# Optimization experiments

Measured on AMD Instinct MI355X. Metric: run time of the kernel, lower is better.

## Reference

```python
import jax, jax.numpy as jnp
import numpy as np

B, W, WIN_IN = 8, 2048, 1024
D, NH, DFF, L, KS = 512, 8, 2048, 4, 4
NGENES, G = 20000, 2048


def _ln(x, g, b, eps=1e-5):
    m = jnp.mean(x, -1, keepdims=True)
    v = jnp.var(x, -1, keepdims=True)
    return (x - m) * jax.lax.rsqrt(v + eps) * g + b


def _mha(q_in, kv_in, qkv_w, qkv_b, out_w, out_b, nh):
    d = q_in.shape[-1]
    hd = d // nh
    wq, wk, wv = qkv_w[:d], qkv_w[d:2 * d], qkv_w[2 * d:]
    bq, bk, bv = qkv_b[:d], qkv_b[d:2 * d], qkv_b[2 * d:]
    q = (q_in @ wq.T + bq).reshape(q_in.shape[0], q_in.shape[1], nh, hd)
    k = (kv_in @ wk.T + bk).reshape(kv_in.shape[0], kv_in.shape[1], nh, hd)
    v = (kv_in @ wv.T + bv).reshape(kv_in.shape[0], kv_in.shape[1], nh, hd)
    scores = jnp.einsum('bqhd,bkhd->bhqk', q, k) / jnp.sqrt(jnp.asarray(hd, q.dtype))
    a = jax.nn.softmax(scores, axis=-1)
    o = jnp.einsum('bhqk,bkhd->bqhd', a, v).reshape(q_in.shape[0], q_in.shape[1], d)
    return o @ out_w.T + out_b


def _posenc(S, d, dtype):
    pos = jnp.arange(S, dtype=jnp.float32)[:, None]
    div = jnp.exp(jnp.arange(0, d, 2, dtype=jnp.float32) * (-np.log(10000.0) / d))
    pe = jnp.zeros((S, d), jnp.float32)
    pe = pe.at[:, 0::2].set(jnp.sin(pos * div)).at[:, 1::2].set(jnp.cos(pos * div))
    return pe.astype(dtype)


def setup_inputs():
    key = jax.random.key(0)
    ks_ = jax.random.split(key, 12)

    def n(k, shape, s=0.02):
        return jax.random.normal(k, shape, jnp.float32) * s

    return dict(
        windows=jax.random.normal(ks_[0], (B, W, WIN_IN), jnp.float32),
        gene_ids=jax.random.randint(ks_[1], (G,), 0, NGENES),
        W_window=n(ks_[2], (D, WIN_IN)),
        enc_qkv_w=n(ks_[3], (L, 3 * D, D)),
        enc_qkv_b=jnp.zeros((L, 3 * D), jnp.float32),
        enc_out_w=n(ks_[4], (L, D, D)),
        enc_out_b=jnp.zeros((L, D), jnp.float32),
        enc_ln1_g=jnp.ones((L, D), jnp.float32),
        enc_ln1_b=jnp.zeros((L, D), jnp.float32),
        enc_ln2_g=jnp.ones((L, D), jnp.float32),
        enc_ln2_b=jnp.zeros((L, D), jnp.float32),
        enc_ff1_w=n(ks_[5], (L, DFF, D)),
        enc_ff1_b=jnp.zeros((L, DFF), jnp.float32),
        enc_ff2_w=n(ks_[6], (L, D, DFF)),
        enc_ff2_b=jnp.zeros((L, D), jnp.float32),
        gene_embed=n(ks_[7], (NGENES, D), 1.0),
        ca_qkv_w=n(ks_[8], (3 * D, D)),
        ca_qkv_b=jnp.zeros((3 * D,), jnp.float32),
        ca_out_w=n(ks_[9], (D, D)),
        ca_out_b=jnp.zeros((D,), jnp.float32),
        ro_ln_g=jnp.ones((D,), jnp.float32),
        ro_ln_b=jnp.zeros((D,), jnp.float32),
        ro_w=n(ks_[10], (1, D)),
        ro_b=jnp.zeros((1,), jnp.float32),
    )


def reference(windows, gene_ids, W_window, enc_qkv_w, enc_qkv_b, enc_out_w,
              enc_out_b, enc_ln1_g, enc_ln1_b, enc_ln2_g, enc_ln2_b,
              enc_ff1_w, enc_ff1_b, enc_ff2_w, enc_ff2_b, gene_embed,
              ca_qkv_w, ca_qkv_b, ca_out_w, ca_out_b, ro_ln_g, ro_ln_b,
              ro_w, ro_b):
    # proj_window (Linear, no bias; dropout inactive in eval)
    x = windows @ W_window.T                          # [B, W, D]
    Bn, Wn, _ = x.shape
    # AvgPool1d(kernel=stride=KS) along the window axis
    x = x.reshape(Bn, Wn // KS, KS, D).mean(axis=2)   # [B, S, D]
    S = x.shape[1]
    x = x + _posenc(S, D, x.dtype)[None]
    # pre-LN TransformerEncoder, relu FFN, no final norm
    for i in range(L):
        h = _ln(x, enc_ln1_g[i], enc_ln1_b[i])
        x = x + _mha(h, h, enc_qkv_w[i], enc_qkv_b[i], enc_out_w[i], enc_out_b[i], NH)
        h = _ln(x, enc_ln2_g[i], enc_ln2_b[i])
        x = x + (jax.nn.relu(h @ enc_ff1_w[i].T + enc_ff1_b[i]) @ enc_ff2_w[i].T + enc_ff2_b[i])
    # gene queries -> cross attention over encoded windows
    q = jnp.broadcast_to(gene_embed[gene_ids][None], (Bn, gene_ids.shape[0], D))
    z = _mha(q, x, ca_qkv_w, ca_qkv_b, ca_out_w, ca_out_b, NH)   # [B, G, D]
    pred = (_ln(z, ro_ln_g, ro_ln_b) @ ro_w.T + ro_b)[..., 0]    # [B, G]
    return pred, z
```

## Files before the change

### kernel.cpp

```cpp
#include <hip/hip_runtime.h>
#include <math.h>


typedef __attribute__((ext_vector_type(8))) short short8v;
typedef __attribute__((ext_vector_type(4))) float float4v;
typedef const __attribute__((address_space(1))) void* gas_t;
typedef __attribute__((address_space(3))) void* las_t;

__device__ inline unsigned short f2bf(float f) {
    unsigned int u = __builtin_bit_cast(unsigned int, f);
    return (unsigned short)((u + 0x7fffu + ((u >> 16) & 1u)) >> 16);
}

__device__ inline unsigned cvt_pk_bf16(float lo, float hi) {
    unsigned r;
    asm("v_cvt_pk_bf16_f32 %0, %1, %2" : "=v"(r) : "v"(lo), "v"(hi));
    return r;
}

__global__ __launch_bounds__(256) void cvt_k(const float* __restrict__ src,
                                             unsigned short* __restrict__ dst, int n4)
{
    int i = blockIdx.x * 256 + threadIdx.x;
    if (i >= n4) return;
    float4 v = ((const float4*)src)[i];
    ushort4 o;
    o.x = f2bf(v.x); o.y = f2bf(v.y); o.z = f2bf(v.z); o.w = f2bf(v.w);
    ((ushort4*)dst)[i] = o;
}

__global__ __launch_bounds__(256) void pool_windows_k(const float* __restrict__ win,
                                                      unsigned short* __restrict__ pw)
{
    int idx = blockIdx.x * 256 + threadIdx.x;
    int n = idx >> 8, c4 = (idx & 255) << 2;
    const float* base = win + (size_t)n * 4096 + c4;
    float4 a = *(const float4*)(base);
    float4 b2 = *(const float4*)(base + 1024);
    float4 c = *(const float4*)(base + 2048);
    float4 d = *(const float4*)(base + 3072);
    ushort4 r;
    r.x = f2bf((a.x + b2.x + c.x + d.x) * 0.25f);
    r.y = f2bf((a.y + b2.y + c.y + d.y) * 0.25f);
    r.z = f2bf((a.z + b2.z + c.z + d.z) * 0.25f);
    r.w = f2bf((a.w + b2.w + c.w + d.w) * 0.25f);
    ((ushort4*)pw)[idx] = r;
}

template<int BM, bool BIAS, bool BROW, bool RES, bool RELU, bool POSENC, bool O32, bool O16>
__global__ __launch_bounds__(256) void gemm_bf16_k(
    const unsigned short* __restrict__ A, const unsigned short* __restrict__ Bw,
    const float* __restrict__ bias, const float* __restrict__ Res,
    float* __restrict__ C32, unsigned short* __restrict__ C16,
    int M, int N, int K)
{
    constexpr int WC   = (BM == 128) ? 2 : 4;
    constexpr int NSTEP = 128 / WC;
    constexpr int MFR  = 4;
    constexpr int NFR  = NSTEP / 16;
    __shared__ __align__(16) unsigned short As[BM * 32];
    __shared__ __align__(16) unsigned short Bs[128 * 32];
    const int tid = threadIdx.x;
    const int lane = tid & 63;
    const int n0 = blockIdx.x * 128, m0 = blockIdx.y * BM;
    const int wr = (BM == 128) ? (tid >> 7) : 0;
    const int wc = (tid >> 6) & (WC - 1);
    const unsigned short* gA0 = A + (size_t)(m0 + (tid >> 2)) * K + (tid & 3) * 8;
    const unsigned short* gA1 = A + (size_t)(m0 + (tid >> 2) + 64) * K + (tid & 3) * 8;
    const unsigned short* gB0 = Bw + (size_t)(n0 + (tid >> 2)) * K + (tid & 3) * 8;
    const unsigned short* gB1 = Bw + (size_t)(n0 + (tid >> 2) + 64) * K + (tid & 3) * 8;
    const int r = lane & 15, g = lane >> 4;
    const int aoff = (64 * wr + r) * 32 + g * 8;
    const int boff = (NSTEP * wc + r) * 32 + g * 8;

    float4v acc[MFR][NFR];
    float4v z4 = {0.f, 0.f, 0.f, 0.f};
    #pragma unroll
    for (int i = 0; i < MFR; ++i)
        #pragma unroll
        for (int j = 0; j < NFR; ++j) acc[i][j] = z4;

    for (int k0 = 0; k0 < K; k0 += 32) {
        __builtin_amdgcn_global_load_lds((gas_t)(gA0 + k0), (las_t)(&As[tid * 8]), 16, 0, 0);
        if constexpr (BM == 128)
            __builtin_amdgcn_global_load_lds((gas_t)(gA1 + k0), (las_t)(&As[(tid + 256) * 8]), 16, 0, 0);
        __builtin_amdgcn_global_load_lds((gas_t)(gB0 + k0), (las_t)(&Bs[tid * 8]), 16, 0, 0);
        __builtin_amdgcn_global_load_lds((gas_t)(gB1 + k0), (las_t)(&Bs[(tid + 256) * 8]), 16, 0, 0);
        __syncthreads();
        short8v a[MFR], b[NFR];
        #pragma unroll
        for (int mi = 0; mi < MFR; ++mi) a[mi] = *(const short8v*)&As[aoff + mi * (16 * 32)];
        #pragma unroll
        for (int ni = 0; ni < NFR; ++ni) b[ni] = *(const short8v*)&Bs[boff + ni * (16 * 32)];
        #pragma unroll
        for (int mi = 0; mi < MFR; ++mi)
            #pragma unroll
            for (int ni = 0; ni < NFR; ++ni)
                acc[mi][ni] = __builtin_amdgcn_mfma_f32_16x16x32_bf16(a[mi], b[ni], acc[mi][ni], 0, 0, 0);
        __syncthreads();
    }

    #pragma unroll
    for (int mi = 0; mi < MFR; ++mi) {
        #pragma unroll
        for (int ni = 0; ni < NFR; ++ni) {
            const int row0 = m0 + 64 * wr + 16 * mi + g * 4;
            const int col  = n0 + NSTEP * wc + 16 * ni + r;
            float bv = (BIAS && !BROW) ? bias[col] : 0.f;
            float fr = 0.f;
            if (POSENC) fr = __expf((float)(col & ~1) * -0.01798894600f);
            #pragma unroll
            for (int q = 0; q < 4; ++q) {
                const int row = row0 + q;
                float v = acc[mi][ni][q] + bv;
                if (BIAS && BROW) v += bias[row];
                if (POSENC) {
                    float ang = (float)(row & 511) * fr;
                    v += (col & 1) ? __cosf(ang) : __sinf(ang);
                }
                if (RES) v += Res[(size_t)row * N + col];
                if (RELU) v = fmaxf(v, 0.f);
                if (O32) C32[(size_t)row * N + col] = v;
                if (O16) C16[(size_t)row * N + col] = f2bf(v);
            }
        }
    }
}

__global__ __launch_bounds__(256) void flashb_k(
    const unsigned short* __restrict__ Qp, long long q_bs, int q_rs,
    const unsigned short* __restrict__ Kp, long long k_bs, int k_rs,
    const unsigned short* __restrict__ Vtp, long long v_hs, long long v_bs, int v_rs,
    unsigned short* __restrict__ Op, long long o_bs, int o_rs, int skv)
{
    constexpr float C1 = 0.18033688011112042f;
    __shared__ __align__(16) unsigned short Ks[64 * 72];
    __shared__ __align__(16) unsigned short Vs[64 * 72];
    __shared__ __align__(16) unsigned short Ps[64 * 72];
    const int qt = blockIdx.x, h = blockIdx.y, b = blockIdx.z;
    const unsigned short* Q  = Qp  + (size_t)b * q_bs + (size_t)h * 64;
    const unsigned short* K  = Kp  + (size_t)b * k_bs + (size_t)h * 64;
    const unsigned short* Vt = Vtp + (size_t)h * v_hs + (size_t)b * v_bs;
    unsigned short* O = Op + (size_t)b * o_bs + (size_t)h * 64;
    const int q0 = qt * 64;
    const int tid = threadIdx.x, lane = tid & 63, w = tid >> 6;
    const int r = lane & 15, g = lane >> 4;

    const unsigned short* qrow = Q + (size_t)(q0 + 16 * w + r) * q_rs + g * 8;
    short8v qf0 = *(const short8v*)(qrow);
    short8v qf1 = *(const short8v*)(qrow + 32);

    const int sr0 = tid >> 3, sr1 = sr0 + 32, sc0 = (tid & 7) * 8;
    const unsigned short* Krow0 = K + (size_t)sr0 * k_rs + sc0;
    const unsigned short* Krow1 = K + (size_t)sr1 * k_rs + sc0;
    const unsigned short* Vrow0 = Vt + (size_t)sr0 * v_rs + sc0;
    const unsigned short* Vrow1 = Vt + (size_t)sr1 * v_rs + sc0;

    uint4 pk0 = *(const uint4*)(Krow0);
    uint4 pk1 = *(const uint4*)(Krow1);
    uint4 pv0 = *(const uint4*)(Vrow0);
    uint4 pv1 = *(const uint4*)(Vrow1);

    float4v acc_o[4];
    float4v z4 = {0.f, 0.f, 0.f, 0.f};
    #pragma unroll
    for (int dt = 0; dt < 4; ++dt) acc_o[dt] = z4;
    float m_own = -INFINITY, l_own = 0.f;

    for (int kv0 = 0; kv0 < skv; kv0 += 64) {
        __syncthreads();
        *(uint4*)&Ks[sr0 * 72 + sc0] = pk0;
        *(uint4*)&Ks[sr1 * 72 + sc0] = pk1;
        *(uint4*)&Vs[sr0 * 72 + sc0] = pv0;
        *(uint4*)&Vs[sr1 * 72 + sc0] = pv1;
        __syncthreads();
        const int kvn = kv0 + 64;
        if (kvn < skv) {
            pk0 = *(const uint4*)(Krow0 + (size_t)kvn * k_rs);
            pk1 = *(const uint4*)(Krow1 + (size_t)kvn * k_rs);
            pv0 = *(const uint4*)(Vrow0 + kvn);
            pv1 = *(const uint4*)(Vrow1 + kvn);
        }

        float4v accs[4];
        #pragma unroll
        for (int t = 0; t < 4; ++t) {
            accs[t] = z4;
            short8v kf0 = *(const short8v*)&Ks[(16 * t + r) * 72 + g * 8];
            short8v kf1 = *(const short8v*)&Ks[(16 * t + r) * 72 + 32 + g * 8];
            accs[t] = __builtin_amdgcn_mfma_f32_16x16x32_bf16(kf0, qf0, accs[t], 0, 0, 0);
            accs[t] = __builtin_amdgcn_mfma_f32_16x16x32_bf16(kf1, qf1, accs[t], 0, 0, 0);
        }

        float sm = accs[0][0];
        #pragma unroll
        for (int t = 0; t < 4; ++t)
            #pragma unroll
            for (int j = 0; j < 4; ++j) sm = fmaxf(sm, accs[t][j]);
        sm = fmaxf(sm, __shfl_xor(sm, 16));
        sm = fmaxf(sm, __shfl_xor(sm, 32));

        if (__any(sm > m_own + 64.f)) {
            float mn = fmaxf(m_own, sm);
            float alpha = __builtin_amdgcn_exp2f((m_own - mn) * C1);
            m_own = mn;
            float a0_ = __shfl(alpha, g * 4 + 0);
            float a1_ = __shfl(alpha, g * 4 + 1);
            float a2_ = __shfl(alpha, g * 4 + 2);
            float a3_ = __shfl(alpha, g * 4 + 3);
            #pragma unroll
            for (int dt = 0; dt < 4; ++dt) {
                acc_o[dt][0] *= a0_; acc_o[dt][1] *= a1_;
                acc_o[dt][2] *= a2_; acc_o[dt][3] *= a3_;
            }
            l_own *= alpha;
        }

        const float m2 = m_own * C1;
        float p[4][4];
        float rsum = 0.f;
        #pragma unroll
        for (int t = 0; t < 4; ++t)
            #pragma unroll
            for (int j = 0; j < 4; ++j) {
                float pv = __builtin_amdgcn_exp2f(__builtin_fmaf(accs[t][j], C1, -m2));
                p[t][j] = pv; rsum += pv;
            }
        rsum += __shfl_xor(rsum, 16);
        rsum += __shfl_xor(rsum, 32);
        l_own += rsum;

        #pragma unroll
        for (int t = 0; t < 4; ++t) {
            uint2 uu;
            uu.x = cvt_pk_bf16(p[t][0], p[t][1]);
            uu.y = cvt_pk_bf16(p[t][2], p[t][3]);
            *(uint2*)&Ps[(16 * w + r) * 72 + 16 * t + g * 4] = uu;
        }

        short8v pf0 = *(const short8v*)&Ps[(16 * w + r) * 72 + g * 8];
        short8v pf1 = *(const short8v*)&Ps[(16 * w + r) * 72 + 32 + g * 8];
        #pragma unroll
        for (int dt = 0; dt < 4; ++dt) {
            short8v vf0 = *(const short8v*)&Vs[(16 * dt + r) * 72 + g * 8];
            short8v vf1 = *(const short8v*)&Vs[(16 * dt + r) * 72 + 32 + g * 8];
            acc_o[dt] = __builtin_amdgcn_mfma_f32_16x16x32_bf16(pf0, vf0, acc_o[dt], 0, 0, 0);
            acc_o[dt] = __builtin_amdgcn_mfma_f32_16x16x32_bf16(pf1, vf1, acc_o[dt], 0, 0, 0);
        }
    }

    float il0 = 1.f / __shfl(l_own, g * 4 + 0);
    float il1 = 1.f / __shfl(l_own, g * 4 + 1);
    float il2 = 1.f / __shfl(l_own, g * 4 + 2);
    float il3 = 1.f / __shfl(l_own, g * 4 + 3);
    #pragma unroll
    for (int dt = 0; dt < 4; ++dt) {
        O[(size_t)(q0 + 16 * w + g * 4 + 0) * o_rs + 16 * dt + r] = f2bf(acc_o[dt][0] * il0);
        O[(size_t)(q0 + 16 * w + g * 4 + 1) * o_rs + 16 * dt + r] = f2bf(acc_o[dt][1] * il1);
        O[(size_t)(q0 + 16 * w + g * 4 + 2) * o_rs + 16 * dt + r] = f2bf(acc_o[dt][2] * il2);
        O[(size_t)(q0 + 16 * w + g * 4 + 3) * o_rs + 16 * dt + r] = f2bf(acc_o[dt][3] * il3);
    }
}

__global__ __launch_bounds__(64) void ln_k(const float* __restrict__ X, unsigned short* __restrict__ Y,
                                           const float* __restrict__ g, const float* __restrict__ bt)
{
    int row = blockIdx.x, lane = threadIdx.x;
    const float* x = X + (size_t)row * 512;
    int c0 = lane * 4, c1 = 256 + lane * 4;
    float4 a0 = *(const float4*)&x[c0];
    float4 a1 = *(const float4*)&x[c1];
    float s  = a0.x + a0.y + a0.z + a0.w + a1.x + a1.y + a1.z + a1.w;
    float ss = a0.x * a0.x + a0.y * a0.y + a0.z * a0.z + a0.w * a0.w
             + a1.x * a1.x + a1.y * a1.y + a1.z * a1.z + a1.w * a1.w;
    #pragma unroll
    for (int off = 1; off < 64; off <<= 1) { s += __shfl_xor(s, off); ss += __shfl_xor(ss, off); }
    float mean = s * (1.f / 512.f);
    float var  = ss * (1.f / 512.f) - mean * mean;
    float rs = rsqrtf(var + 1e-5f);
    float4 g0 = *(const float4*)&g[c0], g1 = *(const float4*)&g[c1];
    float4 b0 = *(const float4*)&bt[c0], b1 = *(const float4*)&bt[c1];
    unsigned short* y = Y + (size_t)row * 512;
    ushort4 o0, o1;
    o0.x = f2bf((a0.x - mean) * rs * g0.x + b0.x);  o0.y = f2bf((a0.y - mean) * rs * g0.y + b0.y);
    o0.z = f2bf((a0.z - mean) * rs * g0.z + b0.z);  o0.w = f2bf((a0.w - mean) * rs * g0.w + b0.w);
    o1.x = f2bf((a1.x - mean) * rs * g1.x + b1.x);  o1.y = f2bf((a1.y - mean) * rs * g1.y + b1.y);
    o1.z = f2bf((a1.z - mean) * rs * g1.z + b1.z);  o1.w = f2bf((a1.w - mean) * rs * g1.w + b1.w);
    *(ushort4*)&y[c0] = o0;
    *(ushort4*)&y[c1] = o1;
}

__global__ __launch_bounds__(128) void gather_k(const float* __restrict__ ge, const int* __restrict__ ids,
                                                unsigned short* __restrict__ out)
{
    int gi = blockIdx.x, t = threadIdx.x;
    int id = ids[gi];
    float4 v = *(const float4*)&ge[(size_t)id * 512 + t * 4];
    ushort4 o;
    o.x = f2bf(v.x); o.y = f2bf(v.y); o.z = f2bf(v.z); o.w = f2bf(v.w);
    *(ushort4*)&out[(size_t)gi * 512 + t * 4] = o;
}

__global__ __launch_bounds__(64) void readout_k(const float* __restrict__ Z,
                                                const float* __restrict__ g, const float* __restrict__ bt,
                                                const float* __restrict__ rw, const float* __restrict__ rb,
                                                float* __restrict__ pred)
{
    int row = blockIdx.x, lane = threadIdx.x;
    const float* zr = Z + (size_t)row * 512;
    int c0 = lane * 4, c1 = 256 + lane * 4;
    float4 a0 = *(const float4*)&zr[c0];
    float4 a1 = *(const float4*)&zr[c1];
    float s  = a0.x + a0.y + a0.z + a0.w + a1.x + a1.y + a1.z + a1.w;
    float ss = a0.x * a0.x + a0.y * a0.y + a0.z * a0.z + a0.w * a0.w
             + a1.x * a1.x + a1.y * a1.y + a1.z * a1.z + a1.w * a1.w;
    #pragma unroll
    for (int off = 1; off < 64; off <<= 1) { s += __shfl_xor(s, off); ss += __shfl_xor(ss, off); }
    float mean = s * (1.f / 512.f);
    float var  = ss * (1.f / 512.f) - mean * mean;
    float rs = rsqrtf(var + 1e-5f);
    float4 g0 = *(const float4*)&g[c0], g1 = *(const float4*)&g[c1];
    float4 b0 = *(const float4*)&bt[c0], b1 = *(const float4*)&bt[c1];
    float4 w0 = *(const float4*)&rw[c0], w1 = *(const float4*)&rw[c1];
    float acc = 0.f;
    acc += ((a0.x - mean) * rs * g0.x + b0.x) * w0.x;
    acc += ((a0.y - mean) * rs * g0.y + b0.y) * w0.y;
    acc += ((a0.z - mean) * rs * g0.z + b0.z) * w0.z;
    acc += ((a0.w - mean) * rs * g0.w + b0.w) * w0.w;
    acc += ((a1.x - mean) * rs * g1.x + b1.x) * w1.x;
    acc += ((a1.y - mean) * rs * g1.y + b1.y) * w1.y;
    acc += ((a1.z - mean) * rs * g1.z + b1.z) * w1.z;
    acc += ((a1.w - mean) * rs * g1.w + b1.w) * w1.w;
    #pragma unroll
    for (int off = 1; off < 64; off <<= 1) acc += __shfl_xor(acc, off);
    if (lane == 0) pred[row] = acc + rb[0];
}

extern "C" void kernel_launch(void* const* d_in, const int* in_sizes, int n_in,
                              void* d_out, int out_size, void* d_ws, size_t ws_size,
                              hipStream_t stream)
{
    (void)in_sizes; (void)n_in; (void)out_size; (void)ws_size;
    const float* windows    = (const float*)d_in[0];
    const int*   gene_ids   = (const int*)  d_in[1];
    const float* W_window   = (const float*)d_in[2];
    const float* enc_qkv_w  = (const float*)d_in[3];
    const float* enc_qkv_b  = (const float*)d_in[4];
    const float* enc_out_w  = (const float*)d_in[5];
    const float* enc_out_b  = (const float*)d_in[6];
    const float* enc_ln1_g  = (const float*)d_in[7];
    const float* enc_ln1_b  = (const float*)d_in[8];
    const float* enc_ln2_g  = (const float*)d_in[9];
    const float* enc_ln2_b  = (const float*)d_in[10];
    const float* enc_ff1_w  = (const float*)d_in[11];
    const float* enc_ff1_b  = (const float*)d_in[12];
    const float* enc_ff2_w  = (const float*)d_in[13];
    const float* enc_ff2_b  = (const float*)d_in[14];
    const float* gene_embed = (const float*)d_in[15];
    const float* ca_qkv_w   = (const float*)d_in[16];
    const float* ca_qkv_b   = (const float*)d_in[17];
    const float* ca_out_w   = (const float*)d_in[18];
    const float* ca_out_b   = (const float*)d_in[19];
    const float* ro_ln_g    = (const float*)d_in[20];
    const float* ro_ln_b    = (const float*)d_in[21];
    const float* ro_w       = (const float*)d_in[22];
    const float* ro_b       = (const float*)d_in[23];

    float* pred = (float*)d_out;
    float* z    = pred + (size_t)8 * 2048;

    char* wp = (char*)d_ws;
    float* x = (float*)wp;                       wp += (size_t)4096 * 512 * 4;
    unsigned short* x16   = (unsigned short*)wp; wp += (size_t)4096 * 512 * 2;
    unsigned short* h16   = (unsigned short*)wp; wp += (size_t)4096 * 512 * 2;
    unsigned short* qkv16 = (unsigned short*)wp; wp += (size_t)4096 * 1536 * 2;
    unsigned short* ao16  = (unsigned short*)wp; wp += (size_t)4096 * 512 * 2;
    unsigned short* big16 = (unsigned short*)wp; wp += (size_t)16384 * 512 * 2;
    unsigned short* vt16  = (unsigned short*)wp; wp += (size_t)512 * 4096 * 2;
    unsigned short* wW16     = (unsigned short*)wp; wp += (size_t)512 * 1024 * 2;
    unsigned short* wqkv16   = (unsigned short*)wp; wp += (size_t)4 * 1536 * 512 * 2;
    unsigned short* wout16   = (unsigned short*)wp; wp += (size_t)4 * 512 * 512 * 2;
    unsigned short* wff116   = (unsigned short*)wp; wp += (size_t)4 * 2048 * 512 * 2;
    unsigned short* wff216   = (unsigned short*)wp; wp += (size_t)4 * 512 * 2048 * 2;
    unsigned short* wcaqkv16 = (unsigned short*)wp; wp += (size_t)1536 * 512 * 2;
    unsigned short* wcaout16 = (unsigned short*)wp; wp += (size_t)512 * 512 * 2;
    unsigned short* pw16  = big16;
    unsigned short* ff116 = big16;
    unsigned short* oc16  = big16;
    unsigned short* ge16  = qkv16;
    unsigned short* qg16  = qkv16 + (size_t)2048 * 512;
    unsigned short* kc16  = qkv16 + (size_t)2 * 2048 * 512;

    auto cvt = [&](const float* s, unsigned short* d, int n) {
        cvt_k<<<(n / 4 + 255) / 256, 256, 0, stream>>>(s, d, n / 4);
    };
    cvt(W_window,  wW16,     512 * 1024);
    cvt(enc_qkv_w, wqkv16,   4 * 1536 * 512);
    cvt(enc_out_w, wout16,   4 * 512 * 512);
    cvt(enc_ff1_w, wff116,   4 * 2048 * 512);
    cvt(enc_ff2_w, wff216,   4 * 512 * 2048);
    cvt(ca_qkv_w,  wcaqkv16, 1536 * 512);
    cvt(ca_out_w,  wcaout16, 512 * 512);

    pool_windows_k<<<4096, 256, 0, stream>>>(windows, pw16);
    gemm_bf16_k<64, false, false, false, false, true, true, false><<<dim3(4, 64), 256, 0, stream>>>(
        pw16, wW16, nullptr, nullptr, x, nullptr, 4096, 512, 1024);

    for (int l = 0; l < 4; ++l) {
        const unsigned short* wl = wqkv16 + (size_t)l * 1536 * 512;
        ln_k<<<4096, 64, 0, stream>>>(x, h16, enc_ln1_g + l * 512, enc_ln1_b + l * 512);
        gemm_bf16_k<128, true, false, false, false, false, false, true><<<dim3(8, 32), 256, 0, stream>>>(
            h16, wl, enc_qkv_b + l * 1536, nullptr, nullptr, qkv16, 4096, 1024, 512);
        gemm_bf16_k<64, true, true, false, false, false, false, true><<<dim3(32, 8), 256, 0, stream>>>(
            wl + (size_t)1024 * 512, h16, enc_qkv_b + l * 1536 + 1024, nullptr,
            nullptr, vt16, 512, 4096, 512);
        flashb_k<<<dim3(8, 8, 8), 256, 0, stream>>>(
            qkv16, (long long)512 * 1024, 1024,
            qkv16 + 512, (long long)512 * 1024, 1024,
            vt16, (long long)64 * 4096, 512LL, 4096,
            ao16, (long long)512 * 512, 512, 512);
        gemm_bf16_k<64, true, false, true, false, false, true, false><<<dim3(4, 64), 256, 0, stream>>>(
            ao16, wout16 + (size_t)l * 512 * 512, enc_out_b + l * 512, x, x, nullptr, 4096, 512, 512);
        ln_k<<<4096, 64, 0, stream>>>(x, h16, enc_ln2_g + l * 512, enc_ln2_b + l * 512);
        gemm_bf16_k<128, true, false, false, true, false, false, true><<<dim3(16, 32), 256, 0, stream>>>(
            h16, wff116 + (size_t)l * 2048 * 512, enc_ff1_b + l * 2048, nullptr,
            nullptr, ff116, 4096, 2048, 512);
        if (l == 3)
            gemm_bf16_k<64, true, false, true, false, false, true, true><<<dim3(4, 64), 256, 0, stream>>>(
                ff116, wff216 + (size_t)l * 512 * 2048, enc_ff2_b + l * 512, x, x, x16, 4096, 512, 2048);
        else
            gemm_bf16_k<64, true, false, true, false, false, true, false><<<dim3(4, 64), 256, 0, stream>>>(
                ff116, wff216 + (size_t)l * 512 * 2048, enc_ff2_b + l * 512, x, x, nullptr, 4096, 512, 2048);
    }

    gather_k<<<2048, 128, 0, stream>>>(gene_embed, gene_ids, ge16);
    gemm_bf16_k<64, true, false, false, false, false, false, true><<<dim3(4, 32), 256, 0, stream>>>(
        ge16, wcaqkv16, ca_qkv_b, nullptr, nullptr, qg16, 2048, 512, 512);
    gemm_bf16_k<64, true, false, false, false, false, false, true><<<dim3(4, 64), 256, 0, stream>>>(
        x16, wcaqkv16 + (size_t)512 * 512, ca_qkv_b + 512, nullptr, nullptr, kc16, 4096, 512, 512);
    gemm_bf16_k<64, true, true, false, false, false, false, true><<<dim3(32, 8), 256, 0, stream>>>(
        wcaqkv16 + (size_t)1024 * 512, x16, ca_qkv_b + 1024, nullptr, nullptr, vt16, 512, 4096, 512);
    flashb_k<<<dim3(32, 8, 8), 256, 0, stream>>>(
        qg16, 0LL, 512,
        kc16, (long long)512 * 512, 512,
        vt16, (long long)64 * 4096, 512LL, 4096,
        oc16, (long long)2048 * 512, 512, 512);
    gemm_bf16_k<128, true, false, false, false, false, true, false><<<dim3(4, 128), 256, 0, stream>>>(
        oc16, wcaout16, ca_out_b, nullptr, z, nullptr, 16384, 512, 512);

    readout_k<<<16384, 64, 0, stream>>>(z, ro_ln_g, ro_ln_b, ro_w, ro_b, pred);
}
```

Baseline: 616.5 us.

## Split encoder attention over KV halves with combine, double-buffer LDS via direct loads

Replaces the flash attention kernel with a templated version that stages K/V tiles into double-buffered, XOR-swizzled LDS using direct global-to-LDS loads, and raises wave priority around the MFMA sections. For the encoder self-attention, the KV range is split in two across extra blocks to double the grid. A new combine kernel merges the partial outputs using the saved per-row max and sum. This aims to improve occupancy and latency hiding, at the cost of an extra kernel launch and an extra pass over the partial outputs in memory.

```diff
diff --git a/kernel.cpp b/kernel.cpp
--- a/kernel.cpp
+++ b/kernel.cpp
@@ -119,7 +119,7 @@
                     v += (col & 1) ? __cosf(ang) : __sinf(ang);
                 }
                 if (RES) v += Res[(size_t)row * N + col];
-                if (RELU) v = fmaxf(v, 0.f);
+                if (RELU) v = fmaxf(v, 0.0f);
                 if (O32) C32[(size_t)row * N + col] = v;
                 if (O16) C16[(size_t)row * N + col] = f2bf(v);
             }
@@ -127,39 +127,49 @@
     }
 }
 
-__global__ __launch_bounds__(256) void flashb_k(
+template<bool SPLIT>
+__global__ __launch_bounds__(256) void flashc_k(
     const unsigned short* __restrict__ Qp, long long q_bs, int q_rs,
     const unsigned short* __restrict__ Kp, long long k_bs, int k_rs,
     const unsigned short* __restrict__ Vtp, long long v_hs, long long v_bs, int v_rs,
-    unsigned short* __restrict__ Op, long long o_bs, int o_rs, int skv)
+    unsigned short* __restrict__ Op, long long o_bs, int o_rs,
+    unsigned short* __restrict__ opart, float2* __restrict__ Ml,
+    int nsplit, int nc)
 {
     constexpr float C1 = 0.18033688011112042f;
-    __shared__ __align__(16) unsigned short Ks[64 * 72];
-    __shared__ __align__(16) unsigned short Vs[64 * 72];
-    __shared__ __align__(16) unsigned short Ps[64 * 72];
-    const int qt = blockIdx.x, h = blockIdx.y, b = blockIdx.z;
+    __shared__ __align__(16) unsigned short Kb[2][64 * 64];
+    __shared__ __align__(16) unsigned short Vb[2][64 * 64];
+    __shared__ __align__(16) unsigned short Ps[64 * 64];
+    const int qt = blockIdx.x, h = blockIdx.y, z = blockIdx.z;
+    const int b = z / nsplit, s = z - b * nsplit;
     const unsigned short* Q  = Qp  + (size_t)b * q_bs + (size_t)h * 64;
-    const unsigned short* K  = Kp  + (size_t)b * k_bs + (size_t)h * 64;
-    const unsigned short* Vt = Vtp + (size_t)h * v_hs + (size_t)b * v_bs;
-    unsigned short* O = Op + (size_t)b * o_bs + (size_t)h * 64;
+    const unsigned short* Kg = Kp  + (size_t)b * k_bs + (size_t)h * 64 + (size_t)(s * nc * 64) * k_rs;
+    const unsigned short* Vg = Vtp + (size_t)h * v_hs + (size_t)b * v_bs + (size_t)(s * nc) * 64;
     const int q0 = qt * 64;
     const int tid = threadIdx.x, lane = tid & 63, w = tid >> 6;
     const int r = lane & 15, g = lane >> 4;
+    const int sw8 = (r & 7) * 8;
+    const int cA = (g * 8) ^ sw8;
+    const int cB = ((g + 4) * 8) ^ sw8;
 
     const unsigned short* qrow = Q + (size_t)(q0 + 16 * w + r) * q_rs + g * 8;
     short8v qf0 = *(const short8v*)(qrow);
     short8v qf1 = *(const short8v*)(qrow + 32);
 
-    const int sr0 = tid >> 3, sr1 = sr0 + 32, sc0 = (tid & 7) * 8;
-    const unsigned short* Krow0 = K + (size_t)sr0 * k_rs + sc0;
-    const unsigned short* Krow1 = K + (size_t)sr1 * k_rs + sc0;
-    const unsigned short* Vrow0 = Vt + (size_t)sr0 * v_rs + sc0;
-    const unsigned short* Vrow1 = Vt + (size_t)sr1 * v_rs + sc0;
-
-    uint4 pk0 = *(const uint4*)(Krow0);
-    uint4 pk1 = *(const uint4*)(Krow1);
-    uint4 pv0 = *(const uint4*)(Vrow0);
-    uint4 pv1 = *(const uint4*)(Vrow1);
+    const int r0 = tid >> 3, cc = tid & 7;
+    const int srcc = (cc ^ (r0 & 7)) * 8;
+    auto stage = [&](int bi, int c) {
+        const unsigned short* kc_ = Kg + (size_t)c * 64 * k_rs;
+        const unsigned short* vc_ = Vg + (size_t)c * 64;
+        __builtin_amdgcn_global_load_lds((gas_t)(kc_ + (size_t)r0 * k_rs + srcc),
+                                         (las_t)(&Kb[bi][tid * 8]), 16, 0, 0);
+        __builtin_amdgcn_global_load_lds((gas_t)(kc_ + (size_t)(r0 + 32) * k_rs + srcc),
+                                         (las_t)(&Kb[bi][(tid + 256) * 8]), 16, 0, 0);
+        __builtin_amdgcn_global_load_lds((gas_t)(vc_ + (size_t)r0 * v_rs + srcc),
+                                         (las_t)(&Vb[bi][tid * 8]), 16, 0, 0);
+        __builtin_amdgcn_global_load_lds((gas_t)(vc_ + (size_t)(r0 + 32) * v_rs + srcc),
+                                         (las_t)(&Vb[bi][(tid + 256) * 8]), 16, 0, 0);
+    };
 
     float4v acc_o[4];
     float4v z4 = {0.f, 0.f, 0.f, 0.f};
@@ -167,36 +177,33 @@
     for (int dt = 0; dt < 4; ++dt) acc_o[dt] = z4;
     float m_own = -INFINITY, l_own = 0.f;
 
-    for (int kv0 = 0; kv0 < skv; kv0 += 64) {
-        __syncthreads();
-        *(uint4*)&Ks[sr0 * 72 + sc0] = pk0;
-        *(uint4*)&Ks[sr1 * 72 + sc0] = pk1;
-        *(uint4*)&Vs[sr0 * 72 + sc0] = pv0;
-        *(uint4*)&Vs[sr1 * 72 + sc0] = pv1;
-        __syncthreads();
-        const int kvn = kv0 + 64;
-        if (kvn < skv) {
-            pk0 = *(const uint4*)(Krow0 + (size_t)kvn * k_rs);
-            pk1 = *(const uint4*)(Krow1 + (size_t)kvn * k_rs);
-            pv0 = *(const uint4*)(Vrow0 + kvn);
-            pv1 = *(const uint4*)(Vrow1 + kvn);
-        }
-
+    stage(0, 0);
+    __syncthreads();
+    int buf = 0;
+
+    for (int c = 0; c < nc; ++c) {
+        if (c + 1 < nc) stage(buf ^ 1, c + 1);
+        const unsigned short* KL = Kb[buf];
+        const unsigned short* VL = Vb[buf];
+
+        __builtin_amdgcn_s_setprio(1);
         float4v accs[4];
         #pragma unroll
         for (int t = 0; t < 4; ++t) {
             accs[t] = z4;
-            short8v kf0 = *(const short8v*)&Ks[(16 * t + r) * 72 + g * 8];
-            short8v kf1 = *(const short8v*)&Ks[(16 * t + r) * 72 + 32 + g * 8];
+            const unsigned short* krow = KL + (16 * t + r) * 64;
+            short8v kf0 = *(const short8v*)(krow + cA);
+            short8v kf1 = *(const short8v*)(krow + cB);
             accs[t] = __builtin_amdgcn_mfma_f32_16x16x32_bf16(kf0, qf0, accs[t], 0, 0, 0);
             accs[t] = __builtin_amdgcn_mfma_f32_16x16x32_bf16(kf1, qf1, accs[t], 0, 0, 0);
         }
-
-        float sm = accs[0][0];
-        #pragma unroll
-        for (int t = 0; t < 4; ++t)
-            #pragma unroll
-            for (int j = 0; j < 4; ++j) sm = fmaxf(sm, accs[t][j]);
+        __builtin_amdgcn_s_setprio(0);
+
+        float m0_ = fmaxf(fmaxf(accs[0][0], accs[0][1]), fmaxf(accs[0][2], accs[0][3]));
+        float m1_ = fmaxf(fmaxf(accs[1][0], accs[1][1]), fmaxf(accs[1][2], accs[1][3]));
+        float m2_ = fmaxf(fmaxf(accs[2][0], accs[2][1]), fmaxf(accs[2][2], accs[2][3]));
+        float m3_ = fmaxf(fmaxf(accs[3][0], accs[3][1]), fmaxf(accs[3][2], accs[3][3]));
+        float sm = fmaxf(fmaxf(m0_, m1_), fmaxf(m2_, m3_));
         sm = fmaxf(sm, __shfl_xor(sm, 16));
         sm = fmaxf(sm, __shfl_xor(sm, 32));
 
@@ -216,50 +223,99 @@
             l_own *= alpha;
         }
 
-        const float m2 = m_own * C1;
+        const float m2c = m_own * C1;
         float p[4][4];
         float rsum = 0.f;
         #pragma unroll
         for (int t = 0; t < 4; ++t)
             #pragma unroll
             for (int j = 0; j < 4; ++j) {
-                float pv = __builtin_amdgcn_exp2f(__builtin_fmaf(accs[t][j], C1, -m2));
+                float pv = __builtin_amdgcn_exp2f(__builtin_fmaf(accs[t][j], C1, -m2c));
                 p[t][j] = pv; rsum += pv;
             }
         rsum += __shfl_xor(rsum, 16);
         rsum += __shfl_xor(rsum, 32);
         l_own += rsum;
 
+        const int prow = (16 * w + r) * 64;
         #pragma unroll
         for (int t = 0; t < 4; ++t) {
             uint2 uu;
             uu.x = cvt_pk_bf16(p[t][0], p[t][1]);
             uu.y = cvt_pk_bf16(p[t][2], p[t][3]);
-            *(uint2*)&Ps[(16 * w + r) * 72 + 16 * t + g * 4] = uu;
-        }
-
-        short8v pf0 = *(const short8v*)&Ps[(16 * w + r) * 72 + g * 8];
-        short8v pf1 = *(const short8v*)&Ps[(16 * w + r) * 72 + 32 + g * 8];
+            int pc = (((2 * t + (g >> 1)) * 8) ^ sw8) + (g & 1) * 4;
+            *(uint2*)&Ps[prow + pc] = uu;
+        }
+
+        __builtin_amdgcn_s_setprio(1);
+        short8v pf0 = *(const short8v*)&Ps[prow + cA];
+        short8v pf1 = *(const short8v*)&Ps[prow + cB];
         #pragma unroll
         for (int dt = 0; dt < 4; ++dt) {
-            short8v vf0 = *(const short8v*)&Vs[(16 * dt + r) * 72 + g * 8];
-            short8v vf1 = *(const short8v*)&Vs[(16 * dt + r) * 72 + 32 + g * 8];
+            const unsigned short* vrow = VL + (16 * dt + r) * 64;
+            short8v vf0 = *(const short8v*)(vrow + cA);
+            short8v vf1 = *(const short8v*)(vrow + cB);
             acc_o[dt] = __builtin_amdgcn_mfma_f32_16x16x32_bf16(pf0, vf0, acc_o[dt], 0, 0, 0);
             acc_o[dt] = __builtin_amdgcn_mfma_f32_16x16x32_bf16(pf1, vf1, acc_o[dt], 0, 0, 0);
         }
+        __builtin_amdgcn_s_setprio(0);
+
+        __syncthreads();
+        buf ^= 1;
     }
 
     float il0 = 1.f / __shfl(l_own, g * 4 + 0);
     float il1 = 1.f / __shfl(l_own, g * 4 + 1);
     float il2 = 1.f / __shfl(l_own, g * 4 + 2);
     float il3 = 1.f / __shfl(l_own, g * 4 + 3);
-    #pragma unroll
-    for (int dt = 0; dt < 4; ++dt) {
-        O[(size_t)(q0 + 16 * w + g * 4 + 0) * o_rs + 16 * dt + r] = f2bf(acc_o[dt][0] * il0);
-        O[(size_t)(q0 + 16 * w + g * 4 + 1) * o_rs + 16 * dt + r] = f2bf(acc_o[dt][1] * il1);
-        O[(size_t)(q0 + 16 * w + g * 4 + 2) * o_rs + 16 * dt + r] = f2bf(acc_o[dt][2] * il2);
-        O[(size_t)(q0 + 16 * w + g * 4 + 3) * o_rs + 16 * dt + r] = f2bf(acc_o[dt][3] * il3);
+    if (SPLIT) {
+        unsigned short* Ob = opart + ((size_t)(s * 4096 + b * 512)) * 512 + h * 64;
+        #pragma unroll
+        for (int dt = 0; dt < 4; ++dt) {
+            Ob[(size_t)(q0 + 16 * w + g * 4 + 0) * 512 + 16 * dt + r] = f2bf(acc_o[dt][0] * il0);
+            Ob[(size_t)(q0 + 16 * w + g * 4 + 1) * 512 + 16 * dt + r] = f2bf(acc_o[dt][1] * il1);
+            Ob[(size_t)(q0 + 16 * w + g * 4 + 2) * 512 + 16 * dt + r] = f2bf(acc_o[dt][2] * il2);
+            Ob[(size_t)(q0 + 16 * w + g * 4 + 3) * 512 + 16 * dt + r] = f2bf(acc_o[dt][3] * il3);
+        }
+        if (g == 0)
+            Ml[((size_t)(s * 8 + b) * 8 + h) * 512 + q0 + 16 * w + r] = make_float2(m_own, l_own);
+    } else {
+        unsigned short* O = Op + (size_t)b * o_bs + (size_t)h * 64;
+        #pragma unroll
+        for (int dt = 0; dt < 4; ++dt) {
+            O[(size_t)(q0 + 16 * w + g * 4 + 0) * o_rs + 16 * dt + r] = f2bf(acc_o[dt][0] * il0);
+            O[(size_t)(q0 + 16 * w + g * 4 + 1) * o_rs + 16 * dt + r] = f2bf(acc_o[dt][1] * il1);
+            O[(size_t)(q0 + 16 * w + g * 4 + 2) * o_rs + 16 * dt + r] = f2bf(acc_o[dt][2] * il2);
+            O[(size_t)(q0 + 16 * w + g * 4 + 3) * o_rs + 16 * dt + r] = f2bf(acc_o[dt][3] * il3);
+        }
     }
+}
+
+__global__ __launch_bounds__(256) void combine_k(const unsigned short* __restrict__ opart,
+                                                 const float2* __restrict__ Ml,
+                                                 unsigned short* __restrict__ Oo)
+{
+    constexpr float C1 = 0.18033688011112042f;
+    const int row = blockIdx.x;
+    const int b = row >> 9, srow = row & 511;
+    const int tid = threadIdx.x;
+    const int h = tid >> 5, t = tid & 31;
+    float2 ml0 = Ml[((size_t)(0 * 8 + b) * 8 + h) * 512 + srow];
+    float2 ml1 = Ml[((size_t)(1 * 8 + b) * 8 + h) * 512 + srow];
+    float m  = fmaxf(ml0.x, ml1.x);
+    float e0 = __builtin_amdgcn_exp2f((ml0.x - m) * C1) * ml0.y;
+    float e1 = __builtin_amdgcn_exp2f((ml1.x - m) * C1) * ml1.y;
+    float inv = 1.f / (e0 + e1);
+    float w0 = e0 * inv, w1 = e1 * inv;
+    const int col = h * 64 + t * 2;
+    unsigned u0 = *(const unsigned*)&opart[((size_t)0 * 4096 + row) * 512 + col];
+    unsigned u1 = *(const unsigned*)&opart[((size_t)1 * 4096 + row) * 512 + col];
+    float a0 = __builtin_bit_cast(float, (u0 & 0xffffu) << 16);
+    float a1 = __builtin_bit_cast(float, (u0 >> 16) << 16);
+    float c0 = __builtin_bit_cast(float, (u1 & 0xffffu) << 16);
+    float c1 = __builtin_bit_cast(float, (u1 >> 16) << 16);
+    unsigned out = cvt_pk_bf16(w0 * a0 + w1 * c0, w0 * a1 + w1 * c1);
+    *(unsigned*)&Oo[(size_t)row * 512 + col] = out;
 }
 
 __global__ __launch_bounds__(64) void ln_k(const float* __restrict__ X, unsigned short* __restrict__ Y,
@@ -384,9 +440,11 @@
     unsigned short* wff216   = (unsigned short*)wp; wp += (size_t)4 * 512 * 2048 * 2;
     unsigned short* wcaqkv16 = (unsigned short*)wp; wp += (size_t)1536 * 512 * 2;
     unsigned short* wcaout16 = (unsigned short*)wp; wp += (size_t)512 * 512 * 2;
-    unsigned short* pw16  = big16;
-    unsigned short* ff116 = big16;
-    unsigned short* oc16  = big16;
+    unsigned short* pw16   = big16;
+    unsigned short* ff116  = big16;
+    unsigned short* oc16   = big16;
+    unsigned short* opart16 = big16;
+    float2* mlbuf = (float2*)(big16 + (size_t)2 * 4096 * 512);
     unsigned short* ge16  = qkv16;
     unsigned short* qg16  = qkv16 + (size_t)2048 * 512;
     unsigned short* kc16  = qkv16 + (size_t)2 * 2048 * 512;
@@ -414,11 +472,13 @@
         gemm_bf16_k<64, true, true, false, false, false, false, true><<<dim3(32, 8), 256, 0, stream>>>(
             wl + (size_t)1024 * 512, h16, enc_qkv_b + l * 1536 + 1024, nullptr,
             nullptr, vt16, 512, 4096, 512);
-        flashb_k<<<dim3(8, 8, 8), 256, 0, stream>>>(
+        flashc_k<true><<<dim3(8, 8, 16), 256, 0, stream>>>(
             qkv16, (long long)512 * 1024, 1024,
             qkv16 + 512, (long long)512 * 1024, 1024,
             vt16, (long long)64 * 4096, 512LL, 4096,
-            ao16, (long long)512 * 512, 512, 512);
+            nullptr, 0LL, 0,
+            opart16, mlbuf, 2, 4);
+        combine_k<<<4096, 256, 0, stream>>>(opart16, mlbuf, ao16);
         gemm_bf16_k<64, true, false, true, false, false, true, false><<<dim3(4, 64), 256, 0, stream>>>(
             ao16, wout16 + (size_t)l * 512 * 512, enc_out_b + l * 512, x, x, nullptr, 4096, 512, 512);
         ln_k<<<4096, 64, 0, stream>>>(x, h16, enc_ln2_g + l * 512, enc_ln2_b + l * 512);
@@ -440,11 +500,12 @@
         x16, wcaqkv16 + (size_t)512 * 512, ca_qkv_b + 512, nullptr, nullptr, kc16, 4096, 512, 512);
     gemm_bf16_k<64, true, true, false, false, false, false, true><<<dim3(32, 8), 256, 0, stream>>>(
         wcaqkv16 + (size_t)1024 * 512, x16, ca_qkv_b + 1024, nullptr, nullptr, vt16, 512, 4096, 512);
-    flashb_k<<<dim3(32, 8, 8), 256, 0, stream>>>(
+    flashc_k<false><<<dim3(32, 8, 8), 256, 0, stream>>>(
         qg16, 0LL, 512,
         kc16, (long long)512 * 512, 512,
         vt16, (long long)64 * 4096, 512LL, 4096,
-        oc16, (long long)2048 * 512, 512, 512);
+        oc16, (long long)2048 * 512, 512,
+        nullptr, nullptr, 1, 8);
     gemm_bf16_k<128, true, false, false, false, false, true, false><<<dim3(4, 128), 256, 0, stream>>>(
         oc16, wcaout16, ca_out_b, nullptr, z, nullptr, 16384, 512, 512);
 
```

New measurement: 640.1 us. +3.8%, slower.
